# Kernel tuning notes

Hardware: AMD Instinct MI355X
Metric: run time of the kernel (lower is better)

Reference implementation:

```python
import jax, jax.numpy as jnp
import numpy as np

EPS = 1e-5

def setup_inputs() -> dict:
    key = jax.random.key(0)
    k1, k2 = jax.random.split(key)
    N, D = 8192, 256
    q_features = jax.random.normal(k1, (N, D), dtype=jnp.float32)
    g_features = jax.random.normal(k2, (N, D), dtype=jnp.float32)
    return {"q_features": q_features, "g_features": g_features}

def reference(q_features, g_features):
    # logits[i, j] = q_i . g_j ; original computes row i as g_features @ q_i
    logits = jnp.einsum('id,jd->ij', q_features, g_features)  # [N, N]
    # exp(l_ii)/sum_j exp(l_ij) == softmax row diagonal (stable form, same math)
    probs_diag = jnp.diagonal(jax.nn.softmax(logits, axis=-1))  # [N]
    loss = jnp.mean(-jnp.log(probs_diag + EPS))
    return loss
```

## Files before the change

kernel.cpp:

```cpp
#include <hip/hip_runtime.h>
#include <stdint.h>


#define LOG2E 1.44269504f
#define KOFF  92.3324826f

typedef __attribute__((ext_vector_type(4))) float f32x4;
typedef long long i64;

typedef __attribute__((address_space(1))) const uint32_t gu32;
typedef __attribute__((address_space(3))) uint32_t lu32;

__global__ __launch_bounds__(256) void k_cvt(const float* __restrict__ q,
                                             const float* __restrict__ g,
                                             char* __restrict__ qb,
                                             char* __restrict__ gb) {
    int o = blockIdx.x * 256 + threadIdx.x;
    const float* src = q;
    char* dst = qb;
    float sc = LOG2E;
    if (o >= 262144) { o -= 262144; src = g; dst = gb; sc = 1.0f; }
    int row = o >> 5, slot = o & 31;
    int ks = slot >> 2, quad = slot & 3;
    const float4* sp = (const float4*)(src + row * 256 + slot * 8);
    float4 a = sp[0], b = sp[1];
    uint32_t w0 = __builtin_amdgcn_cvt_pk_fp8_f32(a.x * sc, a.y * sc, 0, false);
    w0 = __builtin_amdgcn_cvt_pk_fp8_f32(a.z * sc, a.w * sc, w0, true);
    uint32_t w1 = __builtin_amdgcn_cvt_pk_fp8_f32(b.x * sc, b.y * sc, 0, false);
    w1 = __builtin_amdgcn_cvt_pk_fp8_f32(b.z * sc, b.w * sc, w1, true);
    int p = row >> 6, cf = (row >> 4) & 3, l15 = row & 15;
    uint2 wv; wv.x = w0; wv.y = w1;
    *(uint2*)(dst + (size_t)p * 16384 + (ks * 4 + cf) * 512 + (quad * 16 + l15) * 8) = wv;
}

__global__ __launch_bounds__(256, 2) void k_main(const char* __restrict__ qb,
                                                 const char* __restrict__ gb,
                                                 float* __restrict__ zpart,
                                                 float* __restrict__ diag) {
    __shared__ char lds[16384];
    const int tid  = threadIdx.x;
    const int wave = tid >> 6;
    const int lane = tid & 63;
    const int l15  = lane & 15;
    const int quad = lane >> 4;
    const int t    = blockIdx.x >> 5;
    const int cs   = blockIdx.x & 31;
    const int rowbase = t * 256 + wave * 64;

    i64 afrag[4][8];
    {
        const char* qp = qb + (size_t)(t * 4 + wave) * 16384 + lane * 8;
#pragma unroll
        for (int rg = 0; rg < 4; ++rg)
#pragma unroll
            for (int ks = 0; ks < 8; ++ks)
                afrag[rg][ks] = *(const i64*)(qp + ((ks * 4 + rg) << 9));
    }

    float zacc[4][4];
#pragma unroll
    for (int rg = 0; rg < 4; ++rg)
#pragma unroll
        for (int r = 0; r < 4; ++r) zacc[rg][r] = 0.f;

    const bool bd = (t == cs);

    for (int jt = 0; jt < 4; ++jt) {
        const char* gp = gb + (size_t)(cs * 4 + jt) * 16384;
#pragma unroll
        for (int i = 0; i < 4; ++i) {
            int c = wave * 4 + i;
            __builtin_amdgcn_global_load_lds(
                (gu32*)(gp + (c << 10) + (lane << 4)),
                (lu32*)(lds + (c << 10)), 16, 0, 0);
        }
        __syncthreads();

        const bool dg = bd && (jt == wave);
#pragma unroll
        for (int cf = 0; cf < 4; ++cf) {
            f32x4 acc[4];
#pragma unroll
            for (int rg = 0; rg < 4; ++rg)
                acc[rg] = (f32x4){-KOFF, -KOFF, -KOFF, -KOFF};
#pragma unroll
            for (int ks = 0; ks < 8; ++ks) {
                i64 b = *(const i64*)(lds + ((ks * 4 + cf) << 9) + lane * 8);
#pragma unroll
                for (int rg = 0; rg < 4; ++rg)
                    acc[rg] = __builtin_amdgcn_mfma_f32_16x16x32_fp8_fp8(
                        afrag[rg][ks], b, acc[rg], 0, 0, 0);
            }
#pragma unroll
            for (int rg = 0; rg < 4; ++rg)
#pragma unroll
                for (int r = 0; r < 4; ++r)
                    zacc[rg][r] += __builtin_amdgcn_exp2f(acc[rg][r]);
            if (dg) {
#pragma unroll
                for (int r = 0; r < 4; ++r)
                    if (quad * 4 + r == l15)
                        diag[rowbase + cf * 16 + l15] = acc[cf][r];
            }
        }
        __syncthreads();
    }

#pragma unroll
    for (int d = 1; d < 16; d <<= 1)
#pragma unroll
        for (int rg = 0; rg < 4; ++rg)
#pragma unroll
            for (int r = 0; r < 4; ++r)
                zacc[rg][r] += __shfl_xor(zacc[rg][r], d, 64);

    if (l15 == 0) {
#pragma unroll
        for (int rg = 0; rg < 4; ++rg)
#pragma unroll
            for (int r = 0; r < 4; ++r)
                zpart[(rowbase + rg * 16 + quad * 4 + r) * 32 + cs] = zacc[rg][r];
    }
}

__global__ __launch_bounds__(256) void k_fin1(const float* __restrict__ zpart,
                                              const float* __restrict__ diag,
                                              float* __restrict__ partial) {
    __shared__ float red[4];
    int r = blockIdx.x * 256 + threadIdx.x;
    const float4* z = (const float4*)(zpart + r * 32);
    float Z = 0.f;
#pragma unroll
    for (int i = 0; i < 8; ++i) {
        float4 a = z[i];
        Z += (a.x + a.y) + (a.z + a.w);
    }
    float p = __builtin_amdgcn_exp2f(diag[r]) / Z;
    float v = -logf(p + 1e-5f);
#pragma unroll
    for (int dd = 1; dd < 64; dd <<= 1) v += __shfl_xor(v, dd, 64);
    if ((threadIdx.x & 63) == 0) red[threadIdx.x >> 6] = v;
    __syncthreads();
    if (threadIdx.x == 0)
        partial[blockIdx.x] = (red[0] + red[1]) + (red[2] + red[3]);
}

__global__ void k_fin2(const float* __restrict__ partial, float* __restrict__ out) {
    float v = (threadIdx.x < 32) ? partial[threadIdx.x] : 0.f;
#pragma unroll
    for (int d = 1; d < 32; d <<= 1) v += __shfl_xor(v, d, 64);
    if (threadIdx.x == 0) out[0] = v * (1.f / 8192.f);
}

extern "C" void kernel_launch(void* const* d_in, const int* in_sizes, int n_in,
                              void* d_out, int out_size, void* d_ws, size_t ws_size,
                              hipStream_t stream) {
    const float* q = (const float*)d_in[0];
    const float* g = (const float*)d_in[1];
    char* ws = (char*)d_ws;
    char*  qb     = ws;
    char*  gb     = ws + (2u << 20);
    float* diag   = (float*)(ws + (4u << 20));
    float* zpart  = (float*)(ws + (4u << 20) + (32u << 10));
    float* partial= (float*)(ws + (4u << 20) + (1056u << 10));
    k_cvt <<<2048, 256, 0, stream>>>(q, g, qb, gb);
    k_main<<<1024, 256, 0, stream>>>(qb, gb, zpart, diag);
    k_fin1<<<32,   256, 0, stream>>>(zpart, diag, partial);
    k_fin2<<<1,     64, 0, stream>>>(partial, (float*)d_out);
    (void)in_sizes; (void)n_in; (void)out_size; (void)ws_size;
}
```

Baseline: 98.23 us.

## Use 16x16x128 scaled FP8 MFMA with double-buffered LDS for g tiles

Replaces the 16x16x32 fp8 MFMA with the gfx950 scaled 16x16x128 f8f6f4 MFMA using unit scales, so each MFMA covers four times the K depth. The conversion kernel writes a new fragment layout with 16-byte lanes to match, and the main kernel double-buffers the g tile in LDS, prefetching the next tile while the current one is computed, with one barrier per iteration instead of two. The cost is twice the LDS per block and a new operand layout that must match the MFMA lane mapping exactly.

After: 219.2 us. +123.2%, slower.

```diff
diff --git a/kernel.cpp b/kernel.cpp
--- a/kernel.cpp
+++ b/kernel.cpp
@@ -4,9 +4,10 @@
 
 #define LOG2E 1.44269504f
 #define KOFF  92.3324826f
+#define SCL1  0x7F7F7F7F
 
 typedef __attribute__((ext_vector_type(4))) float f32x4;
-typedef long long i64;
+typedef __attribute__((ext_vector_type(8))) int   i32x8;
 
 typedef __attribute__((address_space(1))) const uint32_t gu32;
 typedef __attribute__((address_space(3))) uint32_t lu32;
@@ -19,25 +20,30 @@
     const float* src = q;
     char* dst = qb;
     float sc = LOG2E;
-    if (o >= 262144) { o -= 262144; src = g; dst = gb; sc = 1.0f; }
-    int row = o >> 5, slot = o & 31;
-    int ks = slot >> 2, quad = slot & 3;
-    const float4* sp = (const float4*)(src + row * 256 + slot * 8);
-    float4 a = sp[0], b = sp[1];
-    uint32_t w0 = __builtin_amdgcn_cvt_pk_fp8_f32(a.x * sc, a.y * sc, 0, false);
-    w0 = __builtin_amdgcn_cvt_pk_fp8_f32(a.z * sc, a.w * sc, w0, true);
-    uint32_t w1 = __builtin_amdgcn_cvt_pk_fp8_f32(b.x * sc, b.y * sc, 0, false);
-    w1 = __builtin_amdgcn_cvt_pk_fp8_f32(b.z * sc, b.w * sc, w1, true);
+    if (o >= 131072) { o -= 131072; src = g; dst = gb; sc = 1.0f; }
+    int row = o >> 4, seg = o & 15;
+    const float4* sp = (const float4*)(src + row * 256 + seg * 16);
+    float4 f0 = sp[0], f1 = sp[1], f2 = sp[2], f3 = sp[3];
+    uint32_t w0 = __builtin_amdgcn_cvt_pk_fp8_f32(f0.x * sc, f0.y * sc, 0, false);
+    w0 = __builtin_amdgcn_cvt_pk_fp8_f32(f0.z * sc, f0.w * sc, w0, true);
+    uint32_t w1 = __builtin_amdgcn_cvt_pk_fp8_f32(f1.x * sc, f1.y * sc, 0, false);
+    w1 = __builtin_amdgcn_cvt_pk_fp8_f32(f1.z * sc, f1.w * sc, w1, true);
+    uint32_t w2 = __builtin_amdgcn_cvt_pk_fp8_f32(f2.x * sc, f2.y * sc, 0, false);
+    w2 = __builtin_amdgcn_cvt_pk_fp8_f32(f2.z * sc, f2.w * sc, w2, true);
+    uint32_t w3 = __builtin_amdgcn_cvt_pk_fp8_f32(f3.x * sc, f3.y * sc, 0, false);
+    w3 = __builtin_amdgcn_cvt_pk_fp8_f32(f3.z * sc, f3.w * sc, w3, true);
     int p = row >> 6, cf = (row >> 4) & 3, l15 = row & 15;
-    uint2 wv; wv.x = w0; wv.y = w1;
-    *(uint2*)(dst + (size_t)p * 16384 + (ks * 4 + cf) * 512 + (quad * 16 + l15) * 8) = wv;
+    int h = seg >> 3, sub = seg & 1, quad = (seg >> 1) & 3;
+    int lane = quad * 16 + l15;
+    uint4 wv; wv.x = w0; wv.y = w1; wv.z = w2; wv.w = w3;
+    *(uint4*)(dst + (size_t)p * 16384 + (h * 4 + cf) * 2048 + sub * 1024 + lane * 16) = wv;
 }
 
 __global__ __launch_bounds__(256, 2) void k_main(const char* __restrict__ qb,
                                                  const char* __restrict__ gb,
                                                  float* __restrict__ zpart,
                                                  float* __restrict__ diag) {
-    __shared__ char lds[16384];
+    __shared__ char lds[32768];
     const int tid  = threadIdx.x;
     const int wave = tid >> 6;
     const int lane = tid & 63;
@@ -46,15 +52,28 @@
     const int t    = blockIdx.x >> 5;
     const int cs   = blockIdx.x & 31;
     const int rowbase = t * 256 + wave * 64;
+    const char* gp0 = gb + (size_t)(cs * 4) * 16384;
 
-    i64 afrag[4][8];
+#pragma unroll
+    for (int i = 0; i < 4; ++i) {
+        int c = wave * 4 + i;
+        __builtin_amdgcn_global_load_lds(
+            (gu32*)(gp0 + (c << 10) + (lane << 4)),
+            (lu32*)(lds + (c << 10)), 16, 0, 0);
+    }
+
+    i32x8 afrag[4][2];
     {
-        const char* qp = qb + (size_t)(t * 4 + wave) * 16384 + lane * 8;
+        const char* qp = qb + (size_t)(t * 4 + wave) * 16384 + (lane << 4);
 #pragma unroll
         for (int rg = 0; rg < 4; ++rg)
 #pragma unroll
-            for (int ks = 0; ks < 8; ++ks)
-                afrag[rg][ks] = *(const i64*)(qp + ((ks * 4 + rg) << 9));
+            for (int h = 0; h < 2; ++h) {
+                union { uint4 u[2]; i32x8 v; } cv;
+                cv.u[0] = *(const uint4*)(qp + ((h * 4 + rg) << 11));
+                cv.u[1] = *(const uint4*)(qp + ((h * 4 + rg) << 11) + 1024);
+                afrag[rg][h] = cv.v;
+            }
     }
 
     float zacc[4][4];
@@ -66,16 +85,19 @@
     const bool bd = (t == cs);
 
     for (int jt = 0; jt < 4; ++jt) {
-        const char* gp = gb + (size_t)(cs * 4 + jt) * 16384;
+        __syncthreads();
+        if (jt < 3) {
+            const char* gp = gp0 + ((jt + 1) << 14);
+            char* lb = lds + (((jt + 1) & 1) << 14);
 #pragma unroll
-        for (int i = 0; i < 4; ++i) {
-            int c = wave * 4 + i;
-            __builtin_amdgcn_global_load_lds(
-                (gu32*)(gp + (c << 10) + (lane << 4)),
-                (lu32*)(lds + (c << 10)), 16, 0, 0);
+            for (int i = 0; i < 4; ++i) {
+                int c = wave * 4 + i;
+                __builtin_amdgcn_global_load_lds(
+                    (gu32*)(gp + (c << 10) + (lane << 4)),
+                    (lu32*)(lb + (c << 10)), 16, 0, 0);
+            }
         }
-        __syncthreads();
-
+        const char* lb = lds + ((jt & 1) << 14);
         const bool dg = bd && (jt == wave);
 #pragma unroll
         for (int cf = 0; cf < 4; ++cf) {
@@ -84,12 +106,14 @@
             for (int rg = 0; rg < 4; ++rg)
                 acc[rg] = (f32x4){-KOFF, -KOFF, -KOFF, -KOFF};
 #pragma unroll
-            for (int ks = 0; ks < 8; ++ks) {
-                i64 b = *(const i64*)(lds + ((ks * 4 + cf) << 9) + lane * 8);
+            for (int h = 0; h < 2; ++h) {
+                union { uint4 u[2]; i32x8 v; } bv;
+                bv.u[0] = *(const uint4*)(lb + ((h * 4 + cf) << 11) + (lane << 4));
+                bv.u[1] = *(const uint4*)(lb + ((h * 4 + cf) << 11) + 1024 + (lane << 4));
 #pragma unroll
                 for (int rg = 0; rg < 4; ++rg)
-                    acc[rg] = __builtin_amdgcn_mfma_f32_16x16x32_fp8_fp8(
-                        afrag[rg][ks], b, acc[rg], 0, 0, 0);
+                    acc[rg] = __builtin_amdgcn_mfma_scale_f32_16x16x128_f8f6f4(
+                        afrag[rg][h], bv.v, acc[rg], 0, 0, 0, SCL1, 0, SCL1);
             }
 #pragma unroll
             for (int rg = 0; rg < 4; ++rg)
@@ -103,7 +127,6 @@
                         diag[rowbase + cf * 16 + l15] = acc[cf][r];
             }
         }
-        __syncthreads();
     }
 
 #pragma unroll
@@ -163,7 +186,7 @@
     float* diag   = (float*)(ws + (4u << 20));
     float* zpart  = (float*)(ws + (4u << 20) + (32u << 10));
     float* partial= (float*)(ws + (4u << 20) + (1056u << 10));
-    k_cvt <<<2048, 256, 0, stream>>>(q, g, qb, gb);
+    k_cvt <<<1024, 256, 0, stream>>>(q, g, qb, gb);
     k_main<<<1024, 256, 0, stream>>>(qb, gb, zpart, diag);
     k_fin1<<<32,   256, 0, stream>>>(zpart, diag, partial);
     k_fin2<<<1,     64, 0, stream>>>(partial, (float*)d_out);
```
